# Kernel optimization log

Hardware: AMD Instinct MI355X
Metric: run time of the kernel (lower is better)

The kernel has to match this reference:

```python
import jax, jax.numpy as jnp
import numpy as np

H = 16      # num_heads
D = 64      # head_dim
BQ = 64     # block_size_q
BKV = 64    # block_size_kv


def setup_inputs() -> dict:
    key = jax.random.key(0)
    ks = jax.random.split(key, 5)
    B, S, dim = 2, 2048, 1024
    x = jax.random.normal(ks[0], (B, S, dim), dtype=jnp.float32)
    Wq = jax.random.normal(ks[1], (dim, H * D), dtype=jnp.float32) * 0.02
    Wk = jax.random.normal(ks[2], (dim, H * D), dtype=jnp.float32) * 0.02
    Wv = jax.random.normal(ks[3], (dim, H * D), dtype=jnp.float32) * 0.02
    Wo = jax.random.normal(ks[4], (H * D, dim), dtype=jnp.float32) * 0.02
    return {"x": x, "Wq": Wq, "Wk": Wk, "Wv": Wv, "Wo": Wo}


def _flash_tiled(q, k, v, scale):
    # q,k,v: (B, H, S, D). Non-causal tiled attention with online softmax,
    # faithfully replicating the source's per-iteration division by l_new.
    B, nh, S, d = q.shape
    nq, nkv = S // BQ, S // BKV
    qb = q.reshape(B, nh, nq, BQ, d)                       # all q blocks at once (outer loop vectorized)
    kb = k.reshape(B, nh, nkv, BKV, d).transpose(2, 0, 1, 3, 4)  # (nkv, B, H, BKV, D)
    vb = v.reshape(B, nh, nkv, BKV, d).transpose(2, 0, 1, 3, 4)

    o0 = jnp.zeros((B, nh, nq, BQ, d), q.dtype)
    m0 = jnp.full((B, nh, nq, BQ), -jnp.inf, q.dtype)
    l0 = jnp.zeros((B, nh, nq, BQ), q.dtype)

    def step(carry, kv):
        o, m, l = carry
        kj, vj = kv
        s = jnp.einsum('bhnqd,bhkd->bhnqk', qb, kj) * scale   # (B,H,nq,BQ,BKV)
        m_new = jnp.maximum(m, s.max(axis=-1))
        p = jnp.exp(s - m_new[..., None])
        alpha = jnp.exp(m - m_new)
        l_new = alpha * l + p.sum(axis=-1)
        # NOTE: division by l_new every iteration, as in the source module.
        o_new = (alpha[..., None] * o + jnp.einsum('bhnqk,bhkd->bhnqd', p, vj)) / l_new[..., None]
        return (o_new, m_new, l_new), None

    (o, _, _), _ = jax.lax.scan(step, (o0, m0, l0), (kb, vb))
    return o.reshape(B, nh, S, d)


def reference(x, Wq, Wk, Wv, Wo):
    B, S, dim = x.shape
    scale = D ** -0.5
    q = (x @ Wq).reshape(B, S, H, D).transpose(0, 2, 1, 3)
    k = (x @ Wk).reshape(B, S, H, D).transpose(0, 2, 1, 3)
    v = (x @ Wv).reshape(B, S, H, D).transpose(0, 2, 1, 3)
    o = _flash_tiled(q, k, v, scale)                       # (B,H,S,D)
    out = o.transpose(0, 2, 1, 3).reshape(B, S, H * D)
    return out @ Wo
```

## Files before the change

### kernel.cpp

```cpp
#include <hip/hip_runtime.h>
#include <hip/hip_bf16.h>
#include <math.h>

#define BB   2
#define SS   2048
#define DIM  1024
#define NH   16
#define HD   64
#define MTOT (BB * SS)

typedef unsigned short ushortT;
typedef __attribute__((ext_vector_type(8))) short short8v;
typedef __attribute__((ext_vector_type(4))) float float4v;

union FragU { short8v v; unsigned short us[8]; unsigned int u[4]; };

__device__ inline unsigned short f2bf(float x) {
    unsigned u = __builtin_bit_cast(unsigned, x);
    u += 0x7fffu + ((u >> 16) & 1u);
    return (unsigned short)(u >> 16);
}
__device__ inline float bf2f(unsigned short h) {
    unsigned u = ((unsigned)h) << 16;
    return __builtin_bit_cast(float, u);
}
__device__ inline void split_tr(float x, unsigned short& hi, unsigned short& lo) {
    unsigned u = __builtin_bit_cast(unsigned, x);
    hi = (unsigned short)(u >> 16);
    float hf = __builtin_bit_cast(float, u & 0xffff0000u);
    lo = (unsigned short)(__builtin_bit_cast(unsigned, x - hf) >> 16);
}
__device__ inline void split4(const float4& x, short4& hi, short4& lo) {
    unsigned short h0 = f2bf(x.x), h1 = f2bf(x.y), h2 = f2bf(x.z), h3 = f2bf(x.w);
    hi = make_short4((short)h0, (short)h1, (short)h2, (short)h3);
    lo = make_short4((short)f2bf(x.x - bf2f(h0)), (short)f2bf(x.y - bf2f(h1)),
                     (short)f2bf(x.z - bf2f(h2)), (short)f2bf(x.w - bf2f(h3)));
}
__device__ inline void gld_lds16(const void* g, void* l) {
    __builtin_amdgcn_global_load_lds(
        (const __attribute__((address_space(1))) void*)g,
        (__attribute__((address_space(3))) void*)l, 16, 0, 0);
}

__global__ __launch_bounds__(256) void convert_split_kernel(
    const float* __restrict__ in, ushortT* __restrict__ hi, ushortT* __restrict__ lo, int n4)
{
    int t = blockIdx.x * 256 + threadIdx.x;
    if (t < n4) {
        float4 x = ((const float4*)in)[t];
        short4 h, l; split4(x, h, l);
        ((short4*)hi)[t] = h;
        ((short4*)lo)[t] = l;
    }
}

__global__ __launch_bounds__(256) void transpose_split_kernel(
    const float* __restrict__ W0, const float* __restrict__ W1,
    const float* __restrict__ W2, const float* __restrict__ W3,
    ushortT* __restrict__ WtH, ushortT* __restrict__ WtL)
{
    const int z = blockIdx.z;
    const float* __restrict__ W = (z == 0) ? W0 : (z == 1) ? W1 : (z == 2) ? W2 : W3;
    ushortT* H = WtH + (size_t)z * 1024 * 1024;
    ushortT* L = WtL + (size_t)z * 1024 * 1024;

    __shared__ float T[64][65];
    const int k0 = blockIdx.y * 64, n0 = blockIdx.x * 64;
    const int tid = threadIdx.x;
    const int c4 = (tid & 15) * 4;

#pragma unroll
    for (int i = 0; i < 4; i++) {
        int r = (tid >> 4) + 16 * i;
        *(float4*)&T[r][c4] = *(const float4*)(W + (size_t)(k0 + r) * 1024 + n0 + c4);
    }
    __syncthreads();
#pragma unroll
    for (int i = 0; i < 4; i++) {
        int n = (tid >> 4) + 16 * i;
        float4 vv = make_float4(T[c4 + 0][n], T[c4 + 1][n], T[c4 + 2][n], T[c4 + 3][n]);
        short4 h, l; split4(vv, h, l);
        *(short4*)&H[(size_t)(n0 + n) * 1024 + k0 + c4] = h;
        *(short4*)&L[(size_t)(n0 + n) * 1024 + k0 + c4] = l;
    }
}

__global__ __launch_bounds__(256) void kv_convert_kernel(
    const float* __restrict__ kw,
    ushortT* __restrict__ KhG, ushortT* __restrict__ KlG)
{
    const int jb = blockIdx.x, bh = blockIdx.y;
    const int b = bh >> 4, h = bh & 15;

    __shared__ float T[64][68];
    const int tid = threadIdx.x;
    const size_t ibase = (size_t)b * SS * DIM + (size_t)h * HD + (size_t)(jb * 64) * DIM;
    const int c4 = (tid & 15) * 4;
#pragma unroll
    for (int i = 0; i < 4; i++) {
        int r = (tid >> 4) + 16 * i;
        *(float4*)&T[r][c4] = *(const float4*)(kw + ibase + (size_t)r * DIM + c4);
    }
    __syncthreads();

    ushortT* oh = KhG + (size_t)(bh * 32 + jb) * 4096;
    ushortT* ol = KlG + (size_t)(bh * 32 + jb) * 4096;

#pragma unroll
    for (int i = 0; i < 2; i++) {
        const int s = tid + i * 256;
        const int f = s >> 6;
        const int lane = s & 63;
        const int ks = f >> 2, c = f & 3;
        const int qd = lane >> 4, l15 = lane & 15;
        const int kv = c * 16 + l15;
        const int d0 = ks * 32 + qd * 8;
        ushortT hv[8], lv[8];
#pragma unroll
        for (int j = 0; j < 8; j++) split_tr(T[kv][d0 + j], hv[j], lv[j]);
        *(short4*)&oh[s * 8]     = *(short4*)&hv[0];
        *(short4*)&oh[s * 8 + 4] = *(short4*)&hv[4];
        *(short4*)&ol[s * 8]     = *(short4*)&lv[0];
        *(short4*)&ol[s * 8 + 4] = *(short4*)&lv[4];
    }
}

__global__ __launch_bounds__(256, 2) void gemm_bt_split_kernel(
    const ushortT* __restrict__ Ah, const ushortT* __restrict__ Al,
    const ushortT* __restrict__ BtH, const ushortT* __restrict__ BtL,
    float* __restrict__ Y0, float* __restrict__ Y1,
    ushortT* __restrict__ VhG, ushortT* __restrict__ VlG)
{
    const int z = blockIdx.z;
    const ushortT* __restrict__ Bh = BtH + (size_t)z * 1024 * 1024;
    const ushortT* __restrict__ Bl = BtL + (size_t)z * 1024 * 1024;

    const int K = 1024, N = 1024;
    const int m0 = blockIdx.y * 128;
    const int n0 = blockIdx.x * 128;

    __shared__ __align__(16) ushortT AhS[128 * 32];
    __shared__ __align__(16) ushortT AlS[128 * 32];
    __shared__ __align__(16) ushortT BhS[128 * 32];
    __shared__ __align__(16) ushortT BlS[128 * 32];

    const int tid  = threadIdx.x;
    const int wave = tid >> 6, lane = tid & 63;
    const int quad = lane >> 4, l15 = lane & 15;
    const int wm = wave >> 1, wn = wave & 1;

    const int s0 = tid, s1 = tid + 256;
    const int ar0 = s0 >> 2, ak0 = (s0 & 3) * 8;
    const int ar1 = s1 >> 2, ak1 = (s1 & 3) * 8;

    float4v acc[4][4];
#pragma unroll
    for (int i = 0; i < 4; i++)
#pragma unroll
        for (int j = 0; j < 4; j++) acc[i][j] = (float4v){0.f, 0.f, 0.f, 0.f};

    for (int k0 = 0; k0 < K; k0 += 32) {
        __syncthreads();
        gld_lds16(Ah + (size_t)(m0 + ar0) * K + k0 + ak0, &AhS[s0 * 8]);
        gld_lds16(Ah + (size_t)(m0 + ar1) * K + k0 + ak1, &AhS[s1 * 8]);
        gld_lds16(Al + (size_t)(m0 + ar0) * K + k0 + ak0, &AlS[s0 * 8]);
        gld_lds16(Al + (size_t)(m0 + ar1) * K + k0 + ak1, &AlS[s1 * 8]);
        gld_lds16(Bh + (size_t)(n0 + ar0) * K + k0 + ak0, &BhS[s0 * 8]);
        gld_lds16(Bh + (size_t)(n0 + ar1) * K + k0 + ak1, &BhS[s1 * 8]);
        gld_lds16(Bl + (size_t)(n0 + ar0) * K + k0 + ak0, &BlS[s0 * 8]);
        gld_lds16(Bl + (size_t)(n0 + ar1) * K + k0 + ak1, &BlS[s1 * 8]);
        __syncthreads();

        FragU ah[4], al[4], bh[4], bl[4];
#pragma unroll
        for (int t = 0; t < 4; t++) {
            ah[t].v = *(const short8v*)&AhS[(wm * 64 + t * 16 + l15) * 32 + quad * 8];
            al[t].v = *(const short8v*)&AlS[(wm * 64 + t * 16 + l15) * 32 + quad * 8];
            bh[t].v = *(const short8v*)&BhS[(wn * 64 + t * 16 + l15) * 32 + quad * 8];
            bl[t].v = *(const short8v*)&BlS[(wn * 64 + t * 16 + l15) * 32 + quad * 8];
        }
#pragma unroll
        for (int mt = 0; mt < 4; mt++)
#pragma unroll
            for (int nt = 0; nt < 4; nt++) {
                acc[mt][nt] = __builtin_amdgcn_mfma_f32_16x16x32_bf16(ah[mt].v, bh[nt].v, acc[mt][nt], 0, 0, 0);
                acc[mt][nt] = __builtin_amdgcn_mfma_f32_16x16x32_bf16(ah[mt].v, bl[nt].v, acc[mt][nt], 0, 0, 0);
                acc[mt][nt] = __builtin_amdgcn_mfma_f32_16x16x32_bf16(al[mt].v, bh[nt].v, acc[mt][nt], 0, 0, 0);
            }
    }

    if (z == 2) {
        const int b  = m0 >> 11;
        const int jb = ((m0 & 2047) >> 6) + wm;
        const int h  = (n0 >> 6) + wn;
        const size_t tb = (size_t)((b * 16 + h) * 32 + jb) * 4096;
        ushortT* vh = VhG + tb;
        ushortT* vl = VlG + tb;
#pragma unroll
        for (int mt = 0; mt < 4; mt++)
#pragma unroll
            for (int nt = 0; nt < 4; nt++) {
                const int off = ((((mt >> 1) * 4 + nt) * 64 +
                                  ((mt & 1) * 2 + (quad >> 1)) * 16 + l15) * 8) +
                                (quad & 1) * 4;
                float4 vv = make_float4(acc[mt][nt][0], acc[mt][nt][1],
                                        acc[mt][nt][2], acc[mt][nt][3]);
                unsigned short h0, l0, h1, l1, h2, l2, h3, l3;
                split_tr(vv.x, h0, l0); split_tr(vv.y, h1, l1);
                split_tr(vv.z, h2, l2); split_tr(vv.w, h3, l3);
                *(short4*)&vh[off] = make_short4((short)h0, (short)h1, (short)h2, (short)h3);
                *(short4*)&vl[off] = make_short4((short)l0, (short)l1, (short)l2, (short)l3);
            }
    } else {
        float* __restrict__ Y = (z == 0) ? Y0 : Y1;
#pragma unroll
        for (int mt = 0; mt < 4; mt++)
#pragma unroll
            for (int r = 0; r < 4; r++) {
                const int row = m0 + wm * 64 + mt * 16 + quad * 4 + r;
                float* yp = Y + (size_t)row * N + n0 + wn * 64 + l15;
#pragma unroll
                for (int nt = 0; nt < 4; nt++)
                    yp[nt * 16] = acc[mt][nt][r];
            }
    }
}

__global__ __launch_bounds__(256, 2) void attn_mfma_kernel(
    const float* __restrict__ q,
    const ushortT* __restrict__ KhG, const ushortT* __restrict__ KlG,
    const ushortT* __restrict__ VhG, const ushortT* __restrict__ VlG,
    ushortT* __restrict__ Oh, ushortT* __restrict__ Ol)
{
    __shared__ __align__(16) ushortT KhS[4096];
    __shared__ __align__(16) ushortT KlS[4096];
    __shared__ __align__(16) ushortT VhS[4096];
    __shared__ __align__(16) ushortT VlS[4096];
    __shared__ __align__(16) ushortT PW[4][2][2048];

    const int tid  = threadIdx.x;
    const int wave = tid >> 6, lane = tid & 63;
    const int quad = lane >> 4, l15 = lane & 15;
    const int bh = blockIdx.y, b = bh >> 4, h = bh & 15;
    const size_t base = (size_t)b * SS * DIM + (size_t)h * HD;
    const int qs0 = blockIdx.x * 128 + wave * 32;

    const float qscale = 0.125f * 1.4426950408889634f;
    FragU Qh[2][2], Ql[2][2];
#pragma unroll
    for (int rt = 0; rt < 2; rt++) {
        const int qrow = qs0 + rt * 16 + l15;
#pragma unroll
        for (int ks = 0; ks < 2; ks++) {
            const float* p0 = q + base + (size_t)qrow * DIM + ks * 32 + quad * 8;
            float4 a = *(const float4*)(p0);
            float4 c = *(const float4*)(p0 + 4);
            float e[8] = {a.x, a.y, a.z, a.w, c.x, c.y, c.z, c.w};
#pragma unroll
            for (int j = 0; j < 8; j++) {
                float x = e[j] * qscale;
                unsigned short hs = f2bf(x);
                Qh[rt][ks].us[j] = hs;
                Ql[rt][ks].us[j] = f2bf(x - bf2f(hs));
            }
        }
    }

    float4v Oacc[4][2];
#pragma unroll
    for (int dt = 0; dt < 4; dt++)
#pragma unroll
        for (int rt = 0; rt < 2; rt++) Oacc[dt][rt] = (float4v){0.f, 0.f, 0.f, 0.f};

    float m_run[2] = {-INFINITY, -INFINITY};
    float l_run[2] = {0.f, 0.f};

    const int sl0 = wave * 128 + lane, sl1 = sl0 + 64;
    ushortT* ph = &PW[wave][0][0];
    ushortT* pl = &PW[wave][1][0];
    const int pwq = ((quad >> 1) * 16 + l15) * 8 + (quad & 1) * 4;
    const int lane8 = lane * 8;

    for (int jb = 0; jb < 32; jb++) {
        __syncthreads();
        {
            const size_t tb = (size_t)(bh * 32 + jb) * 4096;
            gld_lds16(KhG + tb + sl0 * 8, &KhS[sl0 * 8]);
            gld_lds16(KhG + tb + sl1 * 8, &KhS[sl1 * 8]);
            gld_lds16(KlG + tb + sl0 * 8, &KlS[sl0 * 8]);
            gld_lds16(KlG + tb + sl1 * 8, &KlS[sl1 * 8]);
            gld_lds16(VhG + tb + sl0 * 8, &VhS[sl0 * 8]);
            gld_lds16(VhG + tb + sl1 * 8, &VhS[sl1 * 8]);
            gld_lds16(VlG + tb + sl0 * 8, &VlS[sl0 * 8]);
            gld_lds16(VlG + tb + sl1 * 8, &VlS[sl1 * 8]);
        }
        __syncthreads();

        float4v st[4][2];
#pragma unroll
        for (int mt = 0; mt < 4; mt++)
#pragma unroll
            for (int rt = 0; rt < 2; rt++) st[mt][rt] = (float4v){0.f, 0.f, 0.f, 0.f};

#pragma unroll
        for (int ks = 0; ks < 2; ks++) {
            FragU kh[4], kl[4];
#pragma unroll
            for (int mt = 0; mt < 4; mt++) {
                kh[mt].v = *(const short8v*)&KhS[((ks * 4 + mt) * 64) * 8 + lane8];
                kl[mt].v = *(const short8v*)&KlS[((ks * 4 + mt) * 64) * 8 + lane8];
            }
#pragma unroll
            for (int mt = 0; mt < 4; mt++)
#pragma unroll
                for (int rt = 0; rt < 2; rt++) {
                    st[mt][rt] = __builtin_amdgcn_mfma_f32_16x16x32_bf16(kh[mt].v, Qh[rt][ks].v, st[mt][rt], 0, 0, 0);
                    st[mt][rt] = __builtin_amdgcn_mfma_f32_16x16x32_bf16(kh[mt].v, Ql[rt][ks].v, st[mt][rt], 0, 0, 0);
                    st[mt][rt] = __builtin_amdgcn_mfma_f32_16x16x32_bf16(kl[mt].v, Qh[rt][ks].v, st[mt][rt], 0, 0, 0);
                }
        }

        float oscale[2];
#pragma unroll
        for (int rt = 0; rt < 2; rt++) {
            float v0 = fmaxf(fmaxf(st[0][rt][0], st[0][rt][1]), fmaxf(st[0][rt][2], st[0][rt][3]));
#pragma unroll
            for (int mt = 1; mt < 4; mt++) {
                float v1 = fmaxf(fmaxf(st[mt][rt][0], st[mt][rt][1]), fmaxf(st[mt][rt][2], st[mt][rt][3]));
                v0 = fmaxf(v0, v1);
            }
            v0 = fmaxf(v0, __shfl_xor(v0, 16, 64));
            v0 = fmaxf(v0, __shfl_xor(v0, 32, 64));
            const float mn = fmaxf(m_run[rt], v0);
            const float al = __builtin_amdgcn_exp2f(m_run[rt] - mn);

            float ssum = 0.f;
#pragma unroll
            for (int mt = 0; mt < 4; mt++)
#pragma unroll
                for (int r = 0; r < 4; r++) {
                    const float p = __builtin_amdgcn_exp2f(st[mt][rt][r] - mn);
                    st[mt][rt][r] = p;
                    ssum += p;
                }
            ssum += __shfl_xor(ssum, 16, 64);
            ssum += __shfl_xor(ssum, 32, 64);
            const float ln = al * l_run[rt] + ssum;
            const float inv = __builtin_amdgcn_rcpf(ln);
            oscale[rt] = al * inv;
#pragma unroll
            for (int mt = 0; mt < 4; mt++)
#pragma unroll
                for (int r = 0; r < 4; r++)
                    st[mt][rt][r] *= inv;
            m_run[rt] = mn;
            l_run[rt] = ln;
        }

#pragma unroll
        for (int rt = 0; rt < 2; rt++)
#pragma unroll
            for (int mt = 0; mt < 4; mt++) {
                unsigned u0 = __builtin_bit_cast(unsigned, st[mt][rt][0]);
                unsigned u1 = __builtin_bit_cast(unsigned, st[mt][rt][1]);
                unsigned u2 = __builtin_bit_cast(unsigned, st[mt][rt][2]);
                unsigned u3 = __builtin_bit_cast(unsigned, st[mt][rt][3]);
                unsigned h01 = (u0 >> 16) | (u1 & 0xffff0000u);
                unsigned h23 = (u2 >> 16) | (u3 & 0xffff0000u);
                float d0 = st[mt][rt][0] - __builtin_bit_cast(float, u0 & 0xffff0000u);
                float d1 = st[mt][rt][1] - __builtin_bit_cast(float, u1 & 0xffff0000u);
                float d2 = st[mt][rt][2] - __builtin_bit_cast(float, u2 & 0xffff0000u);
                float d3 = st[mt][rt][3] - __builtin_bit_cast(float, u3 & 0xffff0000u);
                unsigned l01 = (__builtin_bit_cast(unsigned, d0) >> 16) |
                               (__builtin_bit_cast(unsigned, d1) & 0xffff0000u);
                unsigned l23 = (__builtin_bit_cast(unsigned, d2) >> 16) |
                               (__builtin_bit_cast(unsigned, d3) & 0xffff0000u);
                const int idx = ((rt * 2 + (mt >> 1)) * 512 + (mt & 1) * 256) + pwq;
                *(uint2*)&ph[idx] = make_uint2(h01, h23);
                *(uint2*)&pl[idx] = make_uint2(l01, l23);
            }

        FragU Ph[2][2], Pl[2][2];
#pragma unroll
        for (int rt = 0; rt < 2; rt++)
#pragma unroll
            for (int ks = 0; ks < 2; ks++) {
                Ph[rt][ks].v = *(const short8v*)&ph[((rt * 2 + ks) * 64) * 8 + lane8];
                Pl[rt][ks].v = *(const short8v*)&pl[((rt * 2 + ks) * 64) * 8 + lane8];
            }

#pragma unroll
        for (int dt = 0; dt < 4; dt++)
#pragma unroll
            for (int rt = 0; rt < 2; rt++)
#pragma unroll
                for (int r = 0; r < 4; r++)
                    Oacc[dt][rt][r] *= oscale[rt];

#pragma unroll
        for (int ks = 0; ks < 2; ks++)
#pragma unroll
            for (int dt = 0; dt < 4; dt++) {
                FragU vh, vl;
                vh.v = *(const short8v*)&VhS[((ks * 4 + dt) * 64) * 8 + lane8];
                vl.v = *(const short8v*)&VlS[((ks * 4 + dt) * 64) * 8 + lane8];
#pragma unroll
                for (int rt = 0; rt < 2; rt++) {
                    Oacc[dt][rt] = __builtin_amdgcn_mfma_f32_16x16x32_bf16(vh.v, Ph[rt][ks].v, Oacc[dt][rt], 0, 0, 0);
                    Oacc[dt][rt] = __builtin_amdgcn_mfma_f32_16x16x32_bf16(vl.v, Ph[rt][ks].v, Oacc[dt][rt], 0, 0, 0);
                    Oacc[dt][rt] = __builtin_amdgcn_mfma_f32_16x16x32_bf16(vh.v, Pl[rt][ks].v, Oacc[dt][rt], 0, 0, 0);
                }
            }
    }

    float* Pf = (float*)&PW[wave][0][0];
    const int q16 = lane >> 2, c = lane & 3;
#pragma unroll
    for (int rt = 0; rt < 2; rt++) {
#pragma unroll
        for (int dt = 0; dt < 4; dt++)
            *(float4v*)&Pf[l15 * 68 + dt * 16 + quad * 4] = Oacc[dt][rt];
        float vals[16];
#pragma unroll
        for (int kk = 0; kk < 4; kk++)
            *(float4v*)&vals[kk * 4] = *(const float4v*)&Pf[q16 * 68 + c * 16 + kk * 4];

        unsigned ho[8], lo8[8];
#pragma unroll
        for (int kk = 0; kk < 8; kk++) {
            unsigned short h0, l0, h1, l1;
            split_tr(vals[2 * kk], h0, l0);
            split_tr(vals[2 * kk + 1], h1, l1);
            ho[kk]  = (unsigned)h0 | ((unsigned)h1 << 16);
            lo8[kk] = (unsigned)l0 | ((unsigned)l1 << 16);
        }
        const int qrow = qs0 + rt * 16 + q16;
        const size_t off = (size_t)(b * SS + qrow) * DIM + h * HD + c * 16;
        *(uint4*)&Oh[off]     = make_uint4(ho[0], ho[1], ho[2], ho[3]);
        *(uint4*)&Oh[off + 8] = make_uint4(ho[4], ho[5], ho[6], ho[7]);
        *(uint4*)&Ol[off]     = make_uint4(lo8[0], lo8[1], lo8[2], lo8[3]);
        *(uint4*)&Ol[off + 8] = make_uint4(lo8[4], lo8[5], lo8[6], lo8[7]);
    }
}

extern "C" void kernel_launch(void* const* d_in, const int* in_sizes, int n_in,
                              void* d_out, int out_size, void* d_ws, size_t ws_size,
                              hipStream_t stream)
{
    const float* x  = (const float*)d_in[0];
    const float* Wq = (const float*)d_in[1];
    const float* Wk = (const float*)d_in[2];
    const float* Wv = (const float*)d_in[3];
    const float* Wo = (const float*)d_in[4];
    float* out = (float*)d_out;

    char* w = (char*)d_ws;
    float*   qw  = (float*)(w);
    float*   kw  = (float*)(w + ((size_t)16 << 20));
    ushortT* VhG = (ushortT*)(w + ((size_t)32 << 20));
    ushortT* VlG = (ushortT*)(w + ((size_t)40 << 20));
    ushortT* XhS = (ushortT*)(w + ((size_t)48 << 20));
    ushortT* XlS = (ushortT*)(w + ((size_t)56 << 20));
    ushortT* WtH = (ushortT*)(w + ((size_t)64 << 20));
    ushortT* WtL = (ushortT*)(w + ((size_t)72 << 20));
    ushortT* KhG = (ushortT*)(w + ((size_t)80 << 20));
    ushortT* KlG = (ushortT*)(w + ((size_t)88 << 20));
    ushortT* OhS = (ushortT*)kw;
    ushortT* OlS = (ushortT*)(w + ((size_t)24 << 20));

    dim3 blk(256);
    const int n4 = MTOT * DIM / 4;

    convert_split_kernel<<<dim3(n4 / 256), blk, 0, stream>>>(x, XhS, XlS, n4);
    transpose_split_kernel<<<dim3(16, 16, 4), blk, 0, stream>>>(Wq, Wk, Wv, Wo, WtH, WtL);

    gemm_bt_split_kernel<<<dim3(8, 32, 3), blk, 0, stream>>>(
        XhS, XlS, WtH, WtL, qw, kw, VhG, VlG);

    kv_convert_kernel<<<dim3(32, 32), blk, 0, stream>>>(kw, KhG, KlG);

    attn_mfma_kernel<<<dim3(16, 32), blk, 0, stream>>>(qw, KhG, KlG, VhG, VlG, OhS, OlS);

    gemm_bt_split_kernel<<<dim3(8, 32, 1), blk, 0, stream>>>(
        OhS, OlS, WtH + (size_t)3 * 1024 * 1024, WtL + (size_t)3 * 1024 * 1024,
        out, nullptr, nullptr, nullptr);
}
```

Measured before the change: 331.1 us.

## Switch attention to 32x32x16 MFMA with register-resident P via permlane32 swap

Rewrites the attention inner loop to use 32x32x16 bf16 MFMAs, one 32-row query tile per wave. The K and V split-layout producers are re-indexed to match the new fragment layout. The P matrix now stays in registers: it is packed with v_cvt_pk_bf16_f32 and redistributed with v_permlane32_swap, so the per-wave LDS staging buffer and its write/read round trip are gone. The smaller LDS footprint lets launch bounds ask for 3 blocks per CU, and the epilogue reuses the K/V shared memory. The risks are higher register pressure from the 16-wide accumulators, possible LDS bank conflicts or misalignment in the stride-33 epilogue reads, and slightly different rounding of P (round-to-nearest instead of truncation).

```diff
diff --git a/kernel.cpp b/kernel.cpp
--- a/kernel.cpp
+++ b/kernel.cpp
@@ -12,6 +12,7 @@
 typedef unsigned short ushortT;
 typedef __attribute__((ext_vector_type(8))) short short8v;
 typedef __attribute__((ext_vector_type(4))) float float4v;
+typedef __attribute__((ext_vector_type(16))) float float16v;
 
 union FragU { short8v v; unsigned short us[8]; unsigned int u[4]; };
 
@@ -40,6 +41,14 @@
     __builtin_amdgcn_global_load_lds(
         (const __attribute__((address_space(1))) void*)g,
         (__attribute__((address_space(3))) void*)l, 16, 0, 0);
+}
+__device__ inline unsigned cvt_pk_bf16(float a, float b) {
+    unsigned r;
+    asm("v_cvt_pk_bf16_f32 %0, %1, %2" : "=v"(r) : "v"(a), "v"(b));
+    return r;
+}
+__device__ inline void permlane32_swap(unsigned &a, unsigned &b) {
+    asm("v_permlane32_swap_b32 %0, %1" : "+v"(a), "+v"(b));
 }
 
 __global__ __launch_bounds__(256) void convert_split_kernel(
@@ -111,10 +120,9 @@
         const int s = tid + i * 256;
         const int f = s >> 6;
         const int lane = s & 63;
-        const int ks = f >> 2, c = f & 3;
-        const int qd = lane >> 4, l15 = lane & 15;
-        const int kv = c * 16 + l15;
-        const int d0 = ks * 32 + qd * 8;
+        const int ds = f >> 1, kvt = f & 1;
+        const int kv = kvt * 32 + (lane & 31);
+        const int d0 = ds * 16 + (lane >> 5) * 8;
         ushortT hv[8], lv[8];
 #pragma unroll
         for (int j = 0; j < 8; j++) split_tr(T[kv][d0 + j], hv[j], lv[j]);
@@ -200,8 +208,8 @@
         for (int mt = 0; mt < 4; mt++)
 #pragma unroll
             for (int nt = 0; nt < 4; nt++) {
-                const int off = ((((mt >> 1) * 4 + nt) * 64 +
-                                  ((mt & 1) * 2 + (quad >> 1)) * 16 + l15) * 8) +
+                const int off = ((((nt >> 1) * 4 + mt) * 64 +
+                                  (quad >> 1) * 32 + (nt & 1) * 16 + l15) * 8) +
                                 (quad & 1) * 4;
                 float4 vv = make_float4(acc[mt][nt][0], acc[mt][nt][1],
                                         acc[mt][nt][2], acc[mt][nt][3]);
@@ -226,33 +234,33 @@
     }
 }
 
-__global__ __launch_bounds__(256, 2) void attn_mfma_kernel(
+__global__ __launch_bounds__(256, 3) void attn_mfma_kernel(
     const float* __restrict__ q,
     const ushortT* __restrict__ KhG, const ushortT* __restrict__ KlG,
     const ushortT* __restrict__ VhG, const ushortT* __restrict__ VlG,
     ushortT* __restrict__ Oh, ushortT* __restrict__ Ol)
 {
-    __shared__ __align__(16) ushortT KhS[4096];
-    __shared__ __align__(16) ushortT KlS[4096];
-    __shared__ __align__(16) ushortT VhS[4096];
-    __shared__ __align__(16) ushortT VlS[4096];
-    __shared__ __align__(16) ushortT PW[4][2][2048];
+    __shared__ __align__(16) ushortT SMEM[16384];
+    ushortT* KhS = SMEM;
+    ushortT* KlS = SMEM + 4096;
+    ushortT* VhS = SMEM + 8192;
+    ushortT* VlS = SMEM + 12288;
 
     const int tid  = threadIdx.x;
     const int wave = tid >> 6, lane = tid & 63;
-    const int quad = lane >> 4, l15 = lane & 15;
+    const int l31 = lane & 31, hi5 = lane >> 5;
     const int bh = blockIdx.y, b = bh >> 4, h = bh & 15;
     const size_t base = (size_t)b * SS * DIM + (size_t)h * HD;
     const int qs0 = blockIdx.x * 128 + wave * 32;
+    const int lane8 = lane * 8;
 
     const float qscale = 0.125f * 1.4426950408889634f;
-    FragU Qh[2][2], Ql[2][2];
-#pragma unroll
-    for (int rt = 0; rt < 2; rt++) {
-        const int qrow = qs0 + rt * 16 + l15;
-#pragma unroll
-        for (int ks = 0; ks < 2; ks++) {
-            const float* p0 = q + base + (size_t)qrow * DIM + ks * 32 + quad * 8;
+    FragU Qh[4], Ql[4];
+    {
+        const int qrow = qs0 + l31;
+#pragma unroll
+        for (int ds = 0; ds < 4; ds++) {
+            const float* p0 = q + base + (size_t)qrow * DIM + ds * 16 + hi5 * 8;
             float4 a = *(const float4*)(p0);
             float4 c = *(const float4*)(p0 + 4);
             float e[8] = {a.x, a.y, a.z, a.w, c.x, c.y, c.z, c.w};
@@ -260,26 +268,22 @@
             for (int j = 0; j < 8; j++) {
                 float x = e[j] * qscale;
                 unsigned short hs = f2bf(x);
-                Qh[rt][ks].us[j] = hs;
-                Ql[rt][ks].us[j] = f2bf(x - bf2f(hs));
+                Qh[ds].us[j] = hs;
+                Ql[ds].us[j] = f2bf(x - bf2f(hs));
             }
         }
     }
 
-    float4v Oacc[4][2];
-#pragma unroll
-    for (int dt = 0; dt < 4; dt++)
-#pragma unroll
-        for (int rt = 0; rt < 2; rt++) Oacc[dt][rt] = (float4v){0.f, 0.f, 0.f, 0.f};
-
-    float m_run[2] = {-INFINITY, -INFINITY};
-    float l_run[2] = {0.f, 0.f};
+    float16v Oacc[2];
+#pragma unroll
+    for (int dt = 0; dt < 2; dt++)
+        Oacc[dt] = (float16v){0.f,0.f,0.f,0.f,0.f,0.f,0.f,0.f,
+                              0.f,0.f,0.f,0.f,0.f,0.f,0.f,0.f};
+
+    float m_run = -INFINITY;
+    float l_run = 0.f;
 
     const int sl0 = wave * 128 + lane, sl1 = sl0 + 64;
-    ushortT* ph = &PW[wave][0][0];
-    ushortT* pl = &PW[wave][1][0];
-    const int pwq = ((quad >> 1) * 16 + l15) * 8 + (quad & 1) * 4;
-    const int lane8 = lane * 8;
 
     for (int jb = 0; jb < 32; jb++) {
         __syncthreads();
@@ -296,134 +300,125 @@
         }
         __syncthreads();
 
-        float4v st[4][2];
-#pragma unroll
-        for (int mt = 0; mt < 4; mt++)
-#pragma unroll
-            for (int rt = 0; rt < 2; rt++) st[mt][rt] = (float4v){0.f, 0.f, 0.f, 0.f};
-
-#pragma unroll
-        for (int ks = 0; ks < 2; ks++) {
-            FragU kh[4], kl[4];
-#pragma unroll
-            for (int mt = 0; mt < 4; mt++) {
-                kh[mt].v = *(const short8v*)&KhS[((ks * 4 + mt) * 64) * 8 + lane8];
-                kl[mt].v = *(const short8v*)&KlS[((ks * 4 + mt) * 64) * 8 + lane8];
-            }
-#pragma unroll
-            for (int mt = 0; mt < 4; mt++)
-#pragma unroll
-                for (int rt = 0; rt < 2; rt++) {
-                    st[mt][rt] = __builtin_amdgcn_mfma_f32_16x16x32_bf16(kh[mt].v, Qh[rt][ks].v, st[mt][rt], 0, 0, 0);
-                    st[mt][rt] = __builtin_amdgcn_mfma_f32_16x16x32_bf16(kh[mt].v, Ql[rt][ks].v, st[mt][rt], 0, 0, 0);
-                    st[mt][rt] = __builtin_amdgcn_mfma_f32_16x16x32_bf16(kl[mt].v, Qh[rt][ks].v, st[mt][rt], 0, 0, 0);
-                }
-        }
-
-        float oscale[2];
-#pragma unroll
-        for (int rt = 0; rt < 2; rt++) {
-            float v0 = fmaxf(fmaxf(st[0][rt][0], st[0][rt][1]), fmaxf(st[0][rt][2], st[0][rt][3]));
-#pragma unroll
-            for (int mt = 1; mt < 4; mt++) {
-                float v1 = fmaxf(fmaxf(st[mt][rt][0], st[mt][rt][1]), fmaxf(st[mt][rt][2], st[mt][rt][3]));
-                v0 = fmaxf(v0, v1);
-            }
-            v0 = fmaxf(v0, __shfl_xor(v0, 16, 64));
-            v0 = fmaxf(v0, __shfl_xor(v0, 32, 64));
-            const float mn = fmaxf(m_run[rt], v0);
-            const float al = __builtin_amdgcn_exp2f(m_run[rt] - mn);
+        float16v st[2];
+#pragma unroll
+        for (int t = 0; t < 2; t++)
+            st[t] = (float16v){0.f,0.f,0.f,0.f,0.f,0.f,0.f,0.f,
+                               0.f,0.f,0.f,0.f,0.f,0.f,0.f,0.f};
+
+#pragma unroll
+        for (int ds = 0; ds < 4; ds++) {
+            FragU kh0, kl0, kh1, kl1;
+            kh0.v = *(const short8v*)&KhS[(ds * 2 + 0) * 512 + lane8];
+            kl0.v = *(const short8v*)&KlS[(ds * 2 + 0) * 512 + lane8];
+            kh1.v = *(const short8v*)&KhS[(ds * 2 + 1) * 512 + lane8];
+            kl1.v = *(const short8v*)&KlS[(ds * 2 + 1) * 512 + lane8];
+            st[0] = __builtin_amdgcn_mfma_f32_32x32x16_bf16(kh0.v, Qh[ds].v, st[0], 0, 0, 0);
+            st[0] = __builtin_amdgcn_mfma_f32_32x32x16_bf16(kh0.v, Ql[ds].v, st[0], 0, 0, 0);
+            st[0] = __builtin_amdgcn_mfma_f32_32x32x16_bf16(kl0.v, Qh[ds].v, st[0], 0, 0, 0);
+            st[1] = __builtin_amdgcn_mfma_f32_32x32x16_bf16(kh1.v, Qh[ds].v, st[1], 0, 0, 0);
+            st[1] = __builtin_amdgcn_mfma_f32_32x32x16_bf16(kh1.v, Ql[ds].v, st[1], 0, 0, 0);
+            st[1] = __builtin_amdgcn_mfma_f32_32x32x16_bf16(kl1.v, Qh[ds].v, st[1], 0, 0, 0);
+        }
+
+        float oscale, inv;
+        {
+            float g[8];
+#pragma unroll
+            for (int t = 0; t < 2; t++)
+#pragma unroll
+                for (int i = 0; i < 4; i++)
+                    g[t * 4 + i] = fmaxf(fmaxf(st[t][4 * i], st[t][4 * i + 1]),
+                                         fmaxf(st[t][4 * i + 2], st[t][4 * i + 3]));
+            float vmax = fmaxf(fmaxf(fmaxf(g[0], g[1]), fmaxf(g[2], g[3])),
+                               fmaxf(fmaxf(g[4], g[5]), fmaxf(g[6], g[7])));
+            vmax = fmaxf(vmax, __shfl_xor(vmax, 32, 64));
+            const float mn = fmaxf(m_run, vmax);
+            const float al = __builtin_amdgcn_exp2f(m_run - mn);
 
             float ssum = 0.f;
 #pragma unroll
-            for (int mt = 0; mt < 4; mt++)
-#pragma unroll
-                for (int r = 0; r < 4; r++) {
-                    const float p = __builtin_amdgcn_exp2f(st[mt][rt][r] - mn);
-                    st[mt][rt][r] = p;
+            for (int t = 0; t < 2; t++)
+#pragma unroll
+                for (int r = 0; r < 16; r++) {
+                    const float p = __builtin_amdgcn_exp2f(st[t][r] - mn);
+                    st[t][r] = p;
                     ssum += p;
                 }
-            ssum += __shfl_xor(ssum, 16, 64);
             ssum += __shfl_xor(ssum, 32, 64);
-            const float ln = al * l_run[rt] + ssum;
-            const float inv = __builtin_amdgcn_rcpf(ln);
-            oscale[rt] = al * inv;
-#pragma unroll
-            for (int mt = 0; mt < 4; mt++)
-#pragma unroll
-                for (int r = 0; r < 4; r++)
-                    st[mt][rt][r] *= inv;
-            m_run[rt] = mn;
-            l_run[rt] = ln;
-        }
-
-#pragma unroll
-        for (int rt = 0; rt < 2; rt++)
-#pragma unroll
-            for (int mt = 0; mt < 4; mt++) {
-                unsigned u0 = __builtin_bit_cast(unsigned, st[mt][rt][0]);
-                unsigned u1 = __builtin_bit_cast(unsigned, st[mt][rt][1]);
-                unsigned u2 = __builtin_bit_cast(unsigned, st[mt][rt][2]);
-                unsigned u3 = __builtin_bit_cast(unsigned, st[mt][rt][3]);
-                unsigned h01 = (u0 >> 16) | (u1 & 0xffff0000u);
-                unsigned h23 = (u2 >> 16) | (u3 & 0xffff0000u);
-                float d0 = st[mt][rt][0] - __builtin_bit_cast(float, u0 & 0xffff0000u);
-                float d1 = st[mt][rt][1] - __builtin_bit_cast(float, u1 & 0xffff0000u);
-                float d2 = st[mt][rt][2] - __builtin_bit_cast(float, u2 & 0xffff0000u);
-                float d3 = st[mt][rt][3] - __builtin_bit_cast(float, u3 & 0xffff0000u);
-                unsigned l01 = (__builtin_bit_cast(unsigned, d0) >> 16) |
-                               (__builtin_bit_cast(unsigned, d1) & 0xffff0000u);
-                unsigned l23 = (__builtin_bit_cast(unsigned, d2) >> 16) |
-                               (__builtin_bit_cast(unsigned, d3) & 0xffff0000u);
-                const int idx = ((rt * 2 + (mt >> 1)) * 512 + (mt & 1) * 256) + pwq;
-                *(uint2*)&ph[idx] = make_uint2(h01, h23);
-                *(uint2*)&pl[idx] = make_uint2(l01, l23);
+            const float ln = al * l_run + ssum;
+            inv = __builtin_amdgcn_rcpf(ln);
+            oscale = al * inv;
+#pragma unroll
+            for (int t = 0; t < 2; t++)
+#pragma unroll
+                for (int r = 0; r < 16; r++)
+                    st[t][r] *= inv;
+            m_run = mn;
+            l_run = ln;
+        }
+
+#pragma unroll
+        for (int dt = 0; dt < 2; dt++)
+#pragma unroll
+            for (int r = 0; r < 16; r++)
+                Oacc[dt][r] *= oscale;
+
+#pragma unroll
+        for (int kvs = 0; kvs < 4; kvs++) {
+            const int kvt = kvs >> 1;
+            const int R = (kvs & 1) * 8;
+            float p0 = st[kvt][R + 0], p1 = st[kvt][R + 1];
+            float p2 = st[kvt][R + 2], p3 = st[kvt][R + 3];
+            float p4 = st[kvt][R + 4], p5 = st[kvt][R + 5];
+            float p6 = st[kvt][R + 6], p7 = st[kvt][R + 7];
+            unsigned X0 = cvt_pk_bf16(p0, p1), X1 = cvt_pk_bf16(p2, p3);
+            unsigned Y0 = cvt_pk_bf16(p4, p5), Y1 = cvt_pk_bf16(p6, p7);
+            float e0 = p0 - __builtin_bit_cast(float, X0 << 16);
+            float e1 = p1 - __builtin_bit_cast(float, X0 & 0xffff0000u);
+            float e2 = p2 - __builtin_bit_cast(float, X1 << 16);
+            float e3 = p3 - __builtin_bit_cast(float, X1 & 0xffff0000u);
+            float e4 = p4 - __builtin_bit_cast(float, Y0 << 16);
+            float e5 = p5 - __builtin_bit_cast(float, Y0 & 0xffff0000u);
+            float e6 = p6 - __builtin_bit_cast(float, Y1 << 16);
+            float e7 = p7 - __builtin_bit_cast(float, Y1 & 0xffff0000u);
+            unsigned Z0 = cvt_pk_bf16(e0, e1), Z1 = cvt_pk_bf16(e2, e3);
+            unsigned W0 = cvt_pk_bf16(e4, e5), W1 = cvt_pk_bf16(e6, e7);
+            permlane32_swap(X0, Y0);
+            permlane32_swap(X1, Y1);
+            permlane32_swap(Z0, W0);
+            permlane32_swap(Z1, W1);
+            FragU Phf, Plf;
+            Phf.u[0] = X0; Phf.u[1] = X1; Phf.u[2] = Y0; Phf.u[3] = Y1;
+            Plf.u[0] = Z0; Plf.u[1] = Z1; Plf.u[2] = W0; Plf.u[3] = W1;
+
+#pragma unroll
+            for (int dt = 0; dt < 2; dt++) {
+                FragU vh, vl;
+                vh.v = *(const short8v*)&VhS[(dt * 4 + kvs) * 512 + lane8];
+                vl.v = *(const short8v*)&VlS[(dt * 4 + kvs) * 512 + lane8];
+                Oacc[dt] = __builtin_amdgcn_mfma_f32_32x32x16_bf16(vh.v, Phf.v, Oacc[dt], 0, 0, 0);
+                Oacc[dt] = __builtin_amdgcn_mfma_f32_32x32x16_bf16(vl.v, Phf.v, Oacc[dt], 0, 0, 0);
+                Oacc[dt] = __builtin_amdgcn_mfma_f32_32x32x16_bf16(vh.v, Plf.v, Oacc[dt], 0, 0, 0);
             }
-
-        FragU Ph[2][2], Pl[2][2];
-#pragma unroll
-        for (int rt = 0; rt < 2; rt++)
-#pragma unroll
-            for (int ks = 0; ks < 2; ks++) {
-                Ph[rt][ks].v = *(const short8v*)&ph[((rt * 2 + ks) * 64) * 8 + lane8];
-                Pl[rt][ks].v = *(const short8v*)&pl[((rt * 2 + ks) * 64) * 8 + lane8];
-            }
-
-#pragma unroll
-        for (int dt = 0; dt < 4; dt++)
-#pragma unroll
-            for (int rt = 0; rt < 2; rt++)
-#pragma unroll
-                for (int r = 0; r < 4; r++)
-                    Oacc[dt][rt][r] *= oscale[rt];
-
-#pragma unroll
-        for (int ks = 0; ks < 2; ks++)
-#pragma unroll
-            for (int dt = 0; dt < 4; dt++) {
-                FragU vh, vl;
-                vh.v = *(const short8v*)&VhS[((ks * 4 + dt) * 64) * 8 + lane8];
-                vl.v = *(const short8v*)&VlS[((ks * 4 + dt) * 64) * 8 + lane8];
-#pragma unroll
-                for (int rt = 0; rt < 2; rt++) {
-                    Oacc[dt][rt] = __builtin_amdgcn_mfma_f32_16x16x32_bf16(vh.v, Ph[rt][ks].v, Oacc[dt][rt], 0, 0, 0);
-                    Oacc[dt][rt] = __builtin_amdgcn_mfma_f32_16x16x32_bf16(vl.v, Ph[rt][ks].v, Oacc[dt][rt], 0, 0, 0);
-                    Oacc[dt][rt] = __builtin_amdgcn_mfma_f32_16x16x32_bf16(vh.v, Pl[rt][ks].v, Oacc[dt][rt], 0, 0, 0);
-                }
-            }
-    }
-
-    float* Pf = (float*)&PW[wave][0][0];
-    const int q16 = lane >> 2, c = lane & 3;
-#pragma unroll
-    for (int rt = 0; rt < 2; rt++) {
-#pragma unroll
-        for (int dt = 0; dt < 4; dt++)
-            *(float4v*)&Pf[l15 * 68 + dt * 16 + quad * 4] = Oacc[dt][rt];
+        }
+    }
+
+    __syncthreads();
+    float* EP = ((float*)SMEM) + wave * 1056;
+    const int qq = lane >> 1, dh = (lane & 1) * 16;
+#pragma unroll
+    for (int dt = 0; dt < 2; dt++) {
+#pragma unroll
+        for (int g = 0; g < 4; g++) {
+            float4 wv = make_float4(Oacc[dt][4 * g + 0], Oacc[dt][4 * g + 1],
+                                    Oacc[dt][4 * g + 2], Oacc[dt][4 * g + 3]);
+            *(float4*)&EP[l31 * 33 + g * 8 + hi5 * 4] = wv;
+        }
         float vals[16];
 #pragma unroll
-        for (int kk = 0; kk < 4; kk++)
-            *(float4v*)&vals[kk * 4] = *(const float4v*)&Pf[q16 * 68 + c * 16 + kk * 4];
+        for (int k4 = 0; k4 < 4; k4++)
+            *(float4*)&vals[k4 * 4] = *(const float4*)&EP[qq * 33 + dh + k4 * 4];
 
         unsigned ho[8], lo8[8];
 #pragma unroll
@@ -434,8 +429,8 @@
             ho[kk]  = (unsigned)h0 | ((unsigned)h1 << 16);
             lo8[kk] = (unsigned)l0 | ((unsigned)l1 << 16);
         }
-        const int qrow = qs0 + rt * 16 + q16;
-        const size_t off = (size_t)(b * SS + qrow) * DIM + h * HD + c * 16;
+        const int qrow = qs0 + qq;
+        const size_t off = (size_t)(b * SS + qrow) * DIM + h * HD + dt * 32 + dh;
         *(uint4*)&Oh[off]     = make_uint4(ho[0], ho[1], ho[2], ho[3]);
         *(uint4*)&Oh[off + 8] = make_uint4(ho[4], ho[5], ho[6], ho[7]);
         *(uint4*)&Ol[off]     = make_uint4(lo8[0], lo8[1], lo8[2], lo8[3]);
```

Measured after the change: 324.1 us. -2.1%, faster.
